# Kernel tuning notes

Measured on AMD Instinct MI355X. Metric: run time of the kernel, lower is better.

Reference implementation:

```python
import jax, jax.numpy as jnp
import numpy as np

IN_FEATURES = 2048
OUT_FEATURES = 2048
LOG_DIM = 11                      # ceil(log2(2048))
BUTTERFLY_DIM = 2 ** LOG_DIM      # 2048
MAX_BLOCKS = BUTTERFLY_DIM // 2   # 1024 (layer 0 has the most blocks)
BATCH = 16384


def setup_inputs() -> dict:
    key = jax.random.key(0)
    ks = jax.random.split(key, 5)
    x = jax.random.normal(ks[0], (BATCH, IN_FEATURES), dtype=jnp.float32)
    # Linear weights stored torch-style: [out, in]
    w_in = jax.random.normal(ks[1], (BUTTERFLY_DIM, IN_FEATURES), dtype=jnp.float32) * 0.02
    w_out = jax.random.normal(ks[2], (OUT_FEATURES, BUTTERFLY_DIM), dtype=jnp.float32) * 0.02
    b_out = jnp.zeros((OUT_FEATURES,), dtype=jnp.float32)
    # Per-stage rotation params: theta = rand*0.01, a=cos(theta), b=sin(theta).
    # Stage l uses num_blocks = BUTTERFLY_DIM // 2^(l+1) entries; pad to MAX_BLOCKS.
    theta = jax.random.uniform(ks[3], (LOG_DIM, MAX_BLOCKS), dtype=jnp.float32) * 0.01
    a_pad = jnp.cos(theta)
    b_pad = jnp.sin(theta)
    return {"x": x, "w_in": w_in, "w_out": w_out, "b_out": b_out,
            "a_pad": a_pad, "b_pad": b_pad}


def _butterfly(x, a_pad, b_pad):
    # x: [B, BUTTERFLY_DIM]
    B = x.shape[0]
    for l in range(LOG_DIM):
        block_size = 2 ** l
        num_blocks = BUTTERFLY_DIM // (2 * block_size)
        a = a_pad[l, :num_blocks][None, :, None]  # [1, nb, 1]
        b = b_pad[l, :num_blocks][None, :, None]
        xv = x.reshape(B, num_blocks, 2, block_size)
        x0 = xv[:, :, 0, :]
        x1 = xv[:, :, 1, :]
        top = a * x0 + b * x1
        bot = -b * x0 + a * x1
        x = jnp.stack([top, bot], axis=2).reshape(B, BUTTERFLY_DIM)
    return x


def reference(x, w_in, w_out, b_out, a_pad, b_pad):
    h = x @ w_in.T                      # [B, BUTTERFLY_DIM]
    h = _butterfly(h, a_pad, b_pad)
    return h @ w_out.T + b_out          # [B, OUT_FEATURES]
```

## Files before the change

kernel.cpp:

```cpp
#include <hip/hip_runtime.h>
#include <hip/hip_bf16.h>

using bf16 = __hip_bfloat16;
using bf16x8 = __attribute__((ext_vector_type(8))) __bf16;
using f32x4 = __attribute__((ext_vector_type(4))) float;

typedef const __attribute__((address_space(1))) void* gas_ptr;
typedef __attribute__((address_space(3))) void* las_ptr;
#define LOAD_LDS16(g, l) \
    __builtin_amdgcn_global_load_lds((gas_ptr)(const void*)(g), (las_ptr)(void*)(l), 16, 0, 0)

#define LOG_DIM 11
#define BDIM 2048
#define NFEAT 2048
#define BATCH 16384

__device__ __forceinline__ void cvt_chunk(const float* __restrict__ x,
                                          bf16* __restrict__ x_bf, int chunk, int tid) {
    #pragma unroll
    for (int it = 0; it < 16; ++it) {
        size_t i = ((size_t)chunk * 16 + it) * 2048 + tid * 8;
        float4 v0 = *(const float4*)(x + i);
        float4 v1 = *(const float4*)(x + i + 4);
        union { bf16 h[8]; int4 v; } u;
        u.h[0] = __float2bfloat16(v0.x); u.h[1] = __float2bfloat16(v0.y);
        u.h[2] = __float2bfloat16(v0.z); u.h[3] = __float2bfloat16(v0.w);
        u.h[4] = __float2bfloat16(v1.x); u.h[5] = __float2bfloat16(v1.y);
        u.h[6] = __float2bfloat16(v1.z); u.h[7] = __float2bfloat16(v1.w);
        *(int4*)(x_bf + i) = u.v;
    }
}

__global__ __launch_bounds__(256) void prep1(const float* __restrict__ w_out,
                                             const float* __restrict__ a_pad,
                                             const float* __restrict__ b_pad,
                                             const float* __restrict__ w_in,
                                             bf16* __restrict__ woutb,
                                             bf16* __restrict__ wint,
                                             const float* __restrict__ x,
                                             bf16* __restrict__ x_bf) {
    __shared__ float v[BDIM];
    __shared__ float tile[32][33];
    const int t = threadIdx.x;
    if (blockIdx.x < 2048) {
        const int o = blockIdx.x;
        const float* row = w_out + (size_t)o * BDIM;
        for (int i = t; i < BDIM / 4; i += 256)
            ((float4*)v)[i] = ((const float4*)row)[i];
        __syncthreads();
        for (int l = LOG_DIM - 1; l >= 0; --l) {
            #pragma unroll
            for (int pp = 0; pp < 4; ++pp) {
                int p = t + pp * 256;
                int j = p >> l;
                int s = p & ((1 << l) - 1);
                int i0 = (j << (l + 1)) | s;
                int i1 = i0 + (1 << l);
                float a = a_pad[l * (BDIM / 2) + j];
                float b = b_pad[l * (BDIM / 2) + j];
                float x0 = v[i0], x1 = v[i1];
                v[i0] = a * x0 - b * x1;
                v[i1] = b * x0 + a * x1;
            }
            __syncthreads();
        }
        union { bf16 h[8]; int4 vv; } u;
        #pragma unroll
        for (int j = 0; j < 8; ++j) u.h[j] = __float2bfloat16(v[t * 8 + j]);
        *(int4*)(woutb + (size_t)o * BDIM + t * 8) = u.vv;
    } else if (blockIdx.x < 6144) {
        const int b = blockIdx.x - 2048;
        const int bx = b & 63, by = b >> 6;
        const int tx = t & 31, ty = t >> 5;
        #pragma unroll
        for (int r = ty; r < 32; r += 8)
            tile[r][tx] = w_in[(size_t)(by * 32 + r) * NFEAT + bx * 32 + tx];
        __syncthreads();
        #pragma unroll
        for (int r = ty; r < 32; r += 8)
            wint[(size_t)(bx * 32 + r) * NFEAT + by * 32 + tx] = __float2bfloat16(tile[tx][r]);
    } else {
        cvt_chunk(x, x_bf, 768 + (blockIdx.x - 6144), t);
    }
}

__global__ __launch_bounds__(256, 2) void prep2(const bf16* __restrict__ Aw,
                                                const bf16* __restrict__ Btw,
                                                bf16* __restrict__ Cpart,
                                                const float* __restrict__ x,
                                                bf16* __restrict__ x_bf) {
    __shared__ bf16 sA[128 * 32];
    __shared__ bf16 sB[128 * 32];
    const int tid = threadIdx.x;

    if (blockIdx.x >= 1024) {
        cvt_chunk(x, x_bf, blockIdx.x - 1024, tid);
        return;
    }

    constexpr int BK = 32, LDA = 2048, KLEN = 512, NN = 2048;
    const int sk = blockIdx.x;
    const int bx = sk & 15, by = (sk >> 4) & 15, kz = sk >> 8;
    const bf16* A = Aw + kz * KLEN;
    const bf16* Bt = Btw + kz * KLEN;
    bf16* C = Cpart + (size_t)kz * NN * NN;

    const int wave = tid >> 6, lane = tid & 63;
    const int wr = wave >> 1, wc = wave & 1;
    const int mBase = by * 128, nBase = bx * 128;

    const int r0 = tid >> 2, c0 = tid & 3;
    const int r1 = (256 + tid) >> 2;

    const bf16* gA0 = A + (size_t)(mBase + r0) * LDA + c0 * 8;
    const bf16* gA1 = A + (size_t)(mBase + r1) * LDA + c0 * 8;
    const bf16* gB0 = Bt + (size_t)(nBase + r0) * LDA + c0 * 8;
    const bf16* gB1 = Bt + (size_t)(nBase + r1) * LDA + c0 * 8;

    char* lA0 = (char*)sA + (wave * 64) * 16;
    char* lA1 = (char*)sA + (256 + wave * 64) * 16;
    char* lB0 = (char*)sB + (wave * 64) * 16;
    char* lB1 = (char*)sB + (256 + wave * 64) * 16;

    f32x4 acc[4][4];
    #pragma unroll
    for (int i = 0; i < 4; ++i)
        #pragma unroll
        for (int j = 0; j < 4; ++j) acc[i][j] = (f32x4){0.f, 0.f, 0.f, 0.f};

    const int aRow = wr * 64 + (lane & 15);
    const int bRow = wc * 64 + (lane & 15);
    const int kOff = (lane >> 4) * 8;

    for (int k0 = 0; k0 < KLEN; k0 += BK) {
        LOAD_LDS16(gA0, lA0);
        LOAD_LDS16(gA1, lA1);
        LOAD_LDS16(gB0, lB0);
        LOAD_LDS16(gB1, lB1);
        gA0 += BK; gA1 += BK; gB0 += BK; gB1 += BK;
        __syncthreads();
        bf16x8 af[4], bfr[4];
        #pragma unroll
        for (int mf = 0; mf < 4; ++mf)
            af[mf] = *reinterpret_cast<const bf16x8*>(&sA[(aRow + mf * 16) * BK + kOff]);
        #pragma unroll
        for (int nf = 0; nf < 4; ++nf)
            bfr[nf] = *reinterpret_cast<const bf16x8*>(&sB[(bRow + nf * 16) * BK + kOff]);
        #pragma unroll
        for (int mf = 0; mf < 4; ++mf)
            #pragma unroll
            for (int nf = 0; nf < 4; ++nf)
                acc[mf][nf] = __builtin_amdgcn_mfma_f32_16x16x32_bf16(
                    af[mf], bfr[nf], acc[mf][nf], 0, 0, 0);
        __syncthreads();
    }

    const int cRow0 = mBase + wr * 64 + (lane >> 4) * 4;
    const int cCol0 = nBase + wc * 64 + (lane & 15);
    #pragma unroll
    for (int mf = 0; mf < 4; ++mf)
        #pragma unroll
        for (int nf = 0; nf < 4; ++nf)
            #pragma unroll
            for (int r = 0; r < 4; ++r)
                C[(size_t)(cRow0 + mf * 16 + r) * NN + cCol0 + nf * 16] =
                    __float2bfloat16(acc[mf][nf][r]);
}

__global__ __launch_bounds__(256) void addcvt4(const bf16* __restrict__ p,
                                               bf16* __restrict__ out) {
    size_t i = ((size_t)blockIdx.x * 256 + threadIdx.x) * 8;
    constexpr size_t STRIDE = (size_t)2048 * 2048;
    float s[8];
    #pragma unroll
    for (int j = 0; j < 8; ++j) s[j] = 0.f;
    #pragma unroll
    for (int z = 0; z < 4; ++z) {
        union { bf16 h[8]; int4 v; } a;
        a.v = *(const int4*)(p + z * STRIDE + i);
        #pragma unroll
        for (int j = 0; j < 8; ++j) s[j] += __bfloat162float(a.h[j]);
    }
    union { bf16 h[8]; int4 v; } o;
    #pragma unroll
    for (int j = 0; j < 8; ++j) o.h[j] = __float2bfloat16(s[j]);
    *(int4*)(out + i) = o.v;
}

#define GK 2048
#define LDS_SLOT 65536
#define LDS_BOFF 32768
#define LDS_KH 16384

__global__ __launch_bounds__(512, 2) void gemm256(const bf16* __restrict__ A,
                                                  const bf16* __restrict__ Bt,
                                                  const float* __restrict__ bias,
                                                  float* __restrict__ C) {
    __shared__ __align__(16) char lds[131072];

    const int tid = threadIdx.x;
    const int wave = tid >> 6, lane = tid & 63;
    const int l15 = lane & 15, kc = lane >> 4;
    const int wm = wave >> 2, wn = wave & 3;

    const int bid = blockIdx.x;
    const int swz = (bid & 7) * 64 + (bid >> 3);
    const int bm = swz >> 3, bn = swz & 7;
    const int mBase = bm * 256, nBase = bn * 256;

    const int c_log = tid ^ ((tid >> 3) & 3);
    const int srow = c_log >> 2, skc = c_log & 3;
    const bf16* gA = A + (size_t)(mBase + srow) * GK + skc * 8;
    const bf16* gB = Bt + (size_t)(nBase + srow) * GK + skc * 8;
    const int stgBase = wave * 1024;

    const int kcx = kc ^ ((l15 >> 1) & 3);
    const int aoff = wm * 8192 + l15 * 64 + kcx * 16;
    const int boff = LDS_BOFF + wn * 4096 + l15 * 64 + kcx * 16;

    f32x4 acc[8][4];
    #pragma unroll
    for (int i = 0; i < 8; ++i)
        #pragma unroll
        for (int j = 0; j < 4; ++j) acc[i][j] = (f32x4){0.f, 0.f, 0.f, 0.f};

    bf16x8 Af[4], Bf[4];

#define STG(GSRC, LDSC, KT, KH) do {                                        \
    const bf16* _g = (GSRC) + (KT) * 64 + (KH) * 32;                        \
    LOAD_LDS16(_g, lds + (LDSC) + stgBase);                                 \
    LOAD_LDS16(_g + (size_t)128 * GK, lds + (LDSC) + stgBase + 8192);       \
} while (0)

#define READP(SLOT, KH, MH, DOB) do {                                       \
    const int _rb = (SLOT) * LDS_SLOT + (KH) * LDS_KH;                      \
    _Pragma("unroll")                                                       \
    for (int _f = 0; _f < 4; ++_f)                                          \
        Af[_f] = *(const bf16x8*)(lds + _rb + aoff + (MH) * 4096 + _f * 1024); \
    if (DOB) {                                                              \
        _Pragma("unroll")                                                   \
        for (int _f = 0; _f < 4; ++_f)                                      \
            Bf[_f] = *(const bf16x8*)(lds + _rb + boff + _f * 1024);        \
    }                                                                       \
} while (0)

    STG(gA, 0 * LDS_SLOT + 0, 0, 0);
    STG(gB, 0 * LDS_SLOT + LDS_BOFF + 0, 0, 0);
    STG(gA, 0 * LDS_SLOT + LDS_KH, 0, 1);
    STG(gB, 0 * LDS_SLOT + LDS_BOFF + LDS_KH, 0, 1);
    STG(gA, 1 * LDS_SLOT + 0, 1, 0);
    STG(gB, 1 * LDS_SLOT + LDS_BOFF + 0, 1, 0);
    STG(gB, 1 * LDS_SLOT + LDS_BOFF + LDS_KH, 1, 1);
    asm volatile("s_waitcnt vmcnt(6)");
    __builtin_amdgcn_s_barrier();

#define PH(S, KH, MH, DOB, SGSRC, SLDS, SKT, SKH, DOVM) do {                \
    READP(S, KH, MH, DOB);                                                  \
    STG(SGSRC, SLDS, SKT, SKH);                                             \
    if (DOVM) asm volatile("s_waitcnt vmcnt(6)");                           \
    __builtin_amdgcn_sched_barrier(0);                                      \
    __builtin_amdgcn_s_barrier();                                           \
    asm volatile("s_waitcnt lgkmcnt(0)");                                   \
    __builtin_amdgcn_sched_barrier(0);                                      \
    __builtin_amdgcn_s_setprio(1);                                          \
    _Pragma("unroll")                                                       \
    for (int _mf = 0; _mf < 4; ++_mf)                                       \
        _Pragma("unroll")                                                   \
        for (int _nf = 0; _nf < 4; ++_nf)                                   \
            acc[(MH) * 4 + _mf][_nf] = __builtin_amdgcn_mfma_f32_16x16x32_bf16( \
                Af[_mf], Bf[_nf], acc[(MH) * 4 + _mf][_nf], 0, 0, 0);       \
    __builtin_amdgcn_s_setprio(0);                                          \
    __builtin_amdgcn_s_barrier();                                           \
} while (0)

    for (int it = 0; it < 16; ++it) {
        const int t0 = 2 * it;
        const int t1 = (t0 + 1) & 31, t2 = (t0 + 2) & 31, t3 = (t0 + 3) & 31;
        PH(0, 0, 0, 1, gA, 1 * LDS_SLOT + LDS_KH,            t1, 1, 0);
        PH(0, 0, 1, 0, gB, 0 * LDS_SLOT + LDS_BOFF,          t2, 0, 0);
        PH(0, 1, 0, 1, gA, 0 * LDS_SLOT + 0,                 t2, 0, 0);
        PH(0, 1, 1, 0, gB, 0 * LDS_SLOT + LDS_BOFF + LDS_KH, t2, 1, 1);
        PH(1, 0, 0, 1, gA, 0 * LDS_SLOT + LDS_KH,            t2, 1, 0);
        PH(1, 0, 1, 0, gB, 1 * LDS_SLOT + LDS_BOFF,          t3, 0, 0);
        PH(1, 1, 0, 1, gA, 1 * LDS_SLOT + 0,                 t3, 0, 0);
        PH(1, 1, 1, 0, gB, 1 * LDS_SLOT + LDS_BOFF + LDS_KH, t3, 1, 1);
    }

    const int cRow0 = mBase + wm * 128 + (lane >> 4) * 4;
    const int cCol0 = nBase + wn * 64 + l15;
    float bv[4];
    #pragma unroll
    for (int nf = 0; nf < 4; ++nf) bv[nf] = bias[cCol0 + nf * 16];
    #pragma unroll
    for (int Mf = 0; Mf < 8; ++Mf)
        #pragma unroll
        for (int nf = 0; nf < 4; ++nf)
            #pragma unroll
            for (int r = 0; r < 4; ++r)
                C[(size_t)(cRow0 + Mf * 16 + r) * GK + cCol0 + nf * 16] =
                    acc[Mf][nf][r] + bv[nf];
#undef PH
#undef READP
#undef STG
}

extern "C" void kernel_launch(void* const* d_in, const int* in_sizes, int n_in,
                              void* d_out, int out_size, void* d_ws, size_t ws_size,
                              hipStream_t stream) {
    const float* x     = (const float*)d_in[0];
    const float* w_in  = (const float*)d_in[1];
    const float* w_out = (const float*)d_in[2];
    const float* b_out = (const float*)d_in[3];
    const float* a_pad = (const float*)d_in[4];
    const float* b_pad = (const float*)d_in[5];
    float* out = (float*)d_out;

    char* ws = (char*)d_ws;
    bf16* x_bf  = (bf16*)ws;
    bf16* woutb = (bf16*)(ws + (size_t)67108864);
    bf16* wint  = (bf16*)(ws + (size_t)75497472);
    bf16* mcomb = (bf16*)(ws + (size_t)83886080);

    bf16* part = (bf16*)d_out;

    prep1<<<dim3(6400), dim3(256), 0, stream>>>(w_out, a_pad, b_pad, w_in,
                                                woutb, wint, x, x_bf);
    prep2<<<dim3(1792), dim3(256), 0, stream>>>(woutb, wint, part, x, x_bf);
    addcvt4<<<dim3(NFEAT * BDIM / (256 * 8)), dim3(256), 0, stream>>>(part, mcomb);
    gemm256<<<dim3((BATCH / 256) * (NFEAT / 256)), dim3(512), 0, stream>>>(
        x_bf, mcomb, b_out, out);
}
```

Measured before the change: 228.0 us.

## Use pipelined 256-tile split-K GEMM for weight combine, move x conversion to prep1

The weight-combination GEMM (2048x2048x2048, split-K by 4) previously ran in a simple 128-tile kernel, sharing its launch with part of the x-to-bf16 conversion. It now uses a copy of the main pipelined 256x256 MFMA kernel with a 3D grid over tiles and K-splits. All of the x conversion moves into prep1. The aim is faster MFMA throughput for the combine step, at the cost of a grid of only 256 blocks and no overlap of the conversion with that GEMM.

```diff
diff --git a/kernel.cpp b/kernel.cpp
--- a/kernel.cpp
+++ b/kernel.cpp
@@ -42,8 +42,10 @@
     __shared__ float v[BDIM];
     __shared__ float tile[32][33];
     const int t = threadIdx.x;
-    if (blockIdx.x < 2048) {
-        const int o = blockIdx.x;
+    if (blockIdx.x < 1024) {
+        cvt_chunk(x, x_bf, blockIdx.x, t);
+    } else if (blockIdx.x < 3072) {
+        const int o = blockIdx.x - 1024;
         const float* row = w_out + (size_t)o * BDIM;
         for (int i = t; i < BDIM / 4; i += 256)
             ((float4*)v)[i] = ((const float4*)row)[i];
@@ -68,8 +70,8 @@
         #pragma unroll
         for (int j = 0; j < 8; ++j) u.h[j] = __float2bfloat16(v[t * 8 + j]);
         *(int4*)(woutb + (size_t)o * BDIM + t * 8) = u.vv;
-    } else if (blockIdx.x < 6144) {
-        const int b = blockIdx.x - 2048;
+    } else {
+        const int b = blockIdx.x - 3072;
         const int bx = b & 63, by = b >> 6;
         const int tx = t & 31, ty = t >> 5;
         #pragma unroll
@@ -79,112 +81,7 @@
         #pragma unroll
         for (int r = ty; r < 32; r += 8)
             wint[(size_t)(bx * 32 + r) * NFEAT + by * 32 + tx] = __float2bfloat16(tile[tx][r]);
-    } else {
-        cvt_chunk(x, x_bf, 768 + (blockIdx.x - 6144), t);
-    }
-}
-
-__global__ __launch_bounds__(256, 2) void prep2(const bf16* __restrict__ Aw,
-                                                const bf16* __restrict__ Btw,
-                                                bf16* __restrict__ Cpart,
-                                                const float* __restrict__ x,
-                                                bf16* __restrict__ x_bf) {
-    __shared__ bf16 sA[128 * 32];
-    __shared__ bf16 sB[128 * 32];
-    const int tid = threadIdx.x;
-
-    if (blockIdx.x >= 1024) {
-        cvt_chunk(x, x_bf, blockIdx.x - 1024, tid);
-        return;
-    }
-
-    constexpr int BK = 32, LDA = 2048, KLEN = 512, NN = 2048;
-    const int sk = blockIdx.x;
-    const int bx = sk & 15, by = (sk >> 4) & 15, kz = sk >> 8;
-    const bf16* A = Aw + kz * KLEN;
-    const bf16* Bt = Btw + kz * KLEN;
-    bf16* C = Cpart + (size_t)kz * NN * NN;
-
-    const int wave = tid >> 6, lane = tid & 63;
-    const int wr = wave >> 1, wc = wave & 1;
-    const int mBase = by * 128, nBase = bx * 128;
-
-    const int r0 = tid >> 2, c0 = tid & 3;
-    const int r1 = (256 + tid) >> 2;
-
-    const bf16* gA0 = A + (size_t)(mBase + r0) * LDA + c0 * 8;
-    const bf16* gA1 = A + (size_t)(mBase + r1) * LDA + c0 * 8;
-    const bf16* gB0 = Bt + (size_t)(nBase + r0) * LDA + c0 * 8;
-    const bf16* gB1 = Bt + (size_t)(nBase + r1) * LDA + c0 * 8;
-
-    char* lA0 = (char*)sA + (wave * 64) * 16;
-    char* lA1 = (char*)sA + (256 + wave * 64) * 16;
-    char* lB0 = (char*)sB + (wave * 64) * 16;
-    char* lB1 = (char*)sB + (256 + wave * 64) * 16;
-
-    f32x4 acc[4][4];
-    #pragma unroll
-    for (int i = 0; i < 4; ++i)
-        #pragma unroll
-        for (int j = 0; j < 4; ++j) acc[i][j] = (f32x4){0.f, 0.f, 0.f, 0.f};
-
-    const int aRow = wr * 64 + (lane & 15);
-    const int bRow = wc * 64 + (lane & 15);
-    const int kOff = (lane >> 4) * 8;
-
-    for (int k0 = 0; k0 < KLEN; k0 += BK) {
-        LOAD_LDS16(gA0, lA0);
-        LOAD_LDS16(gA1, lA1);
-        LOAD_LDS16(gB0, lB0);
-        LOAD_LDS16(gB1, lB1);
-        gA0 += BK; gA1 += BK; gB0 += BK; gB1 += BK;
-        __syncthreads();
-        bf16x8 af[4], bfr[4];
-        #pragma unroll
-        for (int mf = 0; mf < 4; ++mf)
-            af[mf] = *reinterpret_cast<const bf16x8*>(&sA[(aRow + mf * 16) * BK + kOff]);
-        #pragma unroll
-        for (int nf = 0; nf < 4; ++nf)
-            bfr[nf] = *reinterpret_cast<const bf16x8*>(&sB[(bRow + nf * 16) * BK + kOff]);
-        #pragma unroll
-        for (int mf = 0; mf < 4; ++mf)
-            #pragma unroll
-            for (int nf = 0; nf < 4; ++nf)
-                acc[mf][nf] = __builtin_amdgcn_mfma_f32_16x16x32_bf16(
-                    af[mf], bfr[nf], acc[mf][nf], 0, 0, 0);
-        __syncthreads();
-    }
-
-    const int cRow0 = mBase + wr * 64 + (lane >> 4) * 4;
-    const int cCol0 = nBase + wc * 64 + (lane & 15);
-    #pragma unroll
-    for (int mf = 0; mf < 4; ++mf)
-        #pragma unroll
-        for (int nf = 0; nf < 4; ++nf)
-            #pragma unroll
-            for (int r = 0; r < 4; ++r)
-                C[(size_t)(cRow0 + mf * 16 + r) * NN + cCol0 + nf * 16] =
-                    __float2bfloat16(acc[mf][nf][r]);
-}
-
-__global__ __launch_bounds__(256) void addcvt4(const bf16* __restrict__ p,
-                                               bf16* __restrict__ out) {
-    size_t i = ((size_t)blockIdx.x * 256 + threadIdx.x) * 8;
-    constexpr size_t STRIDE = (size_t)2048 * 2048;
-    float s[8];
-    #pragma unroll
-    for (int j = 0; j < 8; ++j) s[j] = 0.f;
-    #pragma unroll
-    for (int z = 0; z < 4; ++z) {
-        union { bf16 h[8]; int4 v; } a;
-        a.v = *(const int4*)(p + z * STRIDE + i);
-        #pragma unroll
-        for (int j = 0; j < 8; ++j) s[j] += __bfloat162float(a.h[j]);
-    }
-    union { bf16 h[8]; int4 v; } o;
-    #pragma unroll
-    for (int j = 0; j < 8; ++j) o.h[j] = __float2bfloat16(s[j]);
-    *(int4*)(out + i) = o.v;
+    }
 }
 
 #define GK 2048
@@ -192,10 +89,9 @@
 #define LDS_BOFF 32768
 #define LDS_KH 16384
 
-__global__ __launch_bounds__(512, 2) void gemm256(const bf16* __restrict__ A,
-                                                  const bf16* __restrict__ Bt,
-                                                  const float* __restrict__ bias,
-                                                  float* __restrict__ C) {
+__global__ __launch_bounds__(512, 2) void gemmM_sk(const bf16* __restrict__ A,
+                                                   const bf16* __restrict__ Bt,
+                                                   bf16* __restrict__ part) {
     __shared__ __align__(16) char lds[131072];
 
     const int tid = threadIdx.x;
@@ -203,15 +99,14 @@
     const int l15 = lane & 15, kc = lane >> 4;
     const int wm = wave >> 2, wn = wave & 3;
 
-    const int bid = blockIdx.x;
-    const int swz = (bid & 7) * 64 + (bid >> 3);
-    const int bm = swz >> 3, bn = swz & 7;
-    const int mBase = bm * 256, nBase = bn * 256;
+    const int mBase = blockIdx.y * 256, nBase = blockIdx.x * 256;
+    const int kz = blockIdx.z;
+    bf16* C = part + (size_t)kz * GK * GK;
 
     const int c_log = tid ^ ((tid >> 3) & 3);
     const int srow = c_log >> 2, skc = c_log & 3;
-    const bf16* gA = A + (size_t)(mBase + srow) * GK + skc * 8;
-    const bf16* gB = Bt + (size_t)(nBase + srow) * GK + skc * 8;
+    const bf16* gA = A + (size_t)(mBase + srow) * GK + kz * 512 + skc * 8;
+    const bf16* gB = Bt + (size_t)(nBase + srow) * GK + kz * 512 + skc * 8;
     const int stgBase = wave * 1024;
 
     const int kcx = kc ^ ((l15 >> 1) & 3);
@@ -273,6 +168,135 @@
     __builtin_amdgcn_s_barrier();                                           \
 } while (0)
 
+    for (int it = 0; it < 4; ++it) {
+        const int t0 = 2 * it;
+        const int t1 = (t0 + 1) & 7, t2 = (t0 + 2) & 7, t3 = (t0 + 3) & 7;
+        PH(0, 0, 0, 1, gA, 1 * LDS_SLOT + LDS_KH,            t1, 1, 0);
+        PH(0, 0, 1, 0, gB, 0 * LDS_SLOT + LDS_BOFF,          t2, 0, 0);
+        PH(0, 1, 0, 1, gA, 0 * LDS_SLOT + 0,                 t2, 0, 0);
+        PH(0, 1, 1, 0, gB, 0 * LDS_SLOT + LDS_BOFF + LDS_KH, t2, 1, 1);
+        PH(1, 0, 0, 1, gA, 0 * LDS_SLOT + LDS_KH,            t2, 1, 0);
+        PH(1, 0, 1, 0, gB, 1 * LDS_SLOT + LDS_BOFF,          t3, 0, 0);
+        PH(1, 1, 0, 1, gA, 1 * LDS_SLOT + 0,                 t3, 0, 0);
+        PH(1, 1, 1, 0, gB, 1 * LDS_SLOT + LDS_BOFF + LDS_KH, t3, 1, 1);
+    }
+
+    const int cRow0 = mBase + wm * 128 + (lane >> 4) * 4;
+    const int cCol0 = nBase + wn * 64 + l15;
+    #pragma unroll
+    for (int Mf = 0; Mf < 8; ++Mf)
+        #pragma unroll
+        for (int nf = 0; nf < 4; ++nf)
+            #pragma unroll
+            for (int r = 0; r < 4; ++r)
+                C[(size_t)(cRow0 + Mf * 16 + r) * GK + cCol0 + nf * 16] =
+                    __float2bfloat16(acc[Mf][nf][r]);
+#undef PH
+#undef READP
+#undef STG
+}
+
+__global__ __launch_bounds__(256) void addcvt4(const bf16* __restrict__ p,
+                                               bf16* __restrict__ out) {
+    size_t i = ((size_t)blockIdx.x * 256 + threadIdx.x) * 8;
+    constexpr size_t STRIDE = (size_t)2048 * 2048;
+    float s[8];
+    #pragma unroll
+    for (int j = 0; j < 8; ++j) s[j] = 0.f;
+    #pragma unroll
+    for (int z = 0; z < 4; ++z) {
+        union { bf16 h[8]; int4 v; } a;
+        a.v = *(const int4*)(p + z * STRIDE + i);
+        #pragma unroll
+        for (int j = 0; j < 8; ++j) s[j] += __bfloat162float(a.h[j]);
+    }
+    union { bf16 h[8]; int4 v; } o;
+    #pragma unroll
+    for (int j = 0; j < 8; ++j) o.h[j] = __float2bfloat16(s[j]);
+    *(int4*)(out + i) = o.v;
+}
+
+__global__ __launch_bounds__(512, 2) void gemm256(const bf16* __restrict__ A,
+                                                  const bf16* __restrict__ Bt,
+                                                  const float* __restrict__ bias,
+                                                  float* __restrict__ C) {
+    __shared__ __align__(16) char lds[131072];
+
+    const int tid = threadIdx.x;
+    const int wave = tid >> 6, lane = tid & 63;
+    const int l15 = lane & 15, kc = lane >> 4;
+    const int wm = wave >> 2, wn = wave & 3;
+
+    const int bid = blockIdx.x;
+    const int swz = (bid & 7) * 64 + (bid >> 3);
+    const int bm = swz >> 3, bn = swz & 7;
+    const int mBase = bm * 256, nBase = bn * 256;
+
+    const int c_log = tid ^ ((tid >> 3) & 3);
+    const int srow = c_log >> 2, skc = c_log & 3;
+    const bf16* gA = A + (size_t)(mBase + srow) * GK + skc * 8;
+    const bf16* gB = Bt + (size_t)(nBase + srow) * GK + skc * 8;
+    const int stgBase = wave * 1024;
+
+    const int kcx = kc ^ ((l15 >> 1) & 3);
+    const int aoff = wm * 8192 + l15 * 64 + kcx * 16;
+    const int boff = LDS_BOFF + wn * 4096 + l15 * 64 + kcx * 16;
+
+    f32x4 acc[8][4];
+    #pragma unroll
+    for (int i = 0; i < 8; ++i)
+        #pragma unroll
+        for (int j = 0; j < 4; ++j) acc[i][j] = (f32x4){0.f, 0.f, 0.f, 0.f};
+
+    bf16x8 Af[4], Bf[4];
+
+#define STG(GSRC, LDSC, KT, KH) do {                                        \
+    const bf16* _g = (GSRC) + (KT) * 64 + (KH) * 32;                        \
+    LOAD_LDS16(_g, lds + (LDSC) + stgBase);                                 \
+    LOAD_LDS16(_g + (size_t)128 * GK, lds + (LDSC) + stgBase + 8192);       \
+} while (0)
+
+#define READP(SLOT, KH, MH, DOB) do {                                       \
+    const int _rb = (SLOT) * LDS_SLOT + (KH) * LDS_KH;                      \
+    _Pragma("unroll")                                                       \
+    for (int _f = 0; _f < 4; ++_f)                                          \
+        Af[_f] = *(const bf16x8*)(lds + _rb + aoff + (MH) * 4096 + _f * 1024); \
+    if (DOB) {                                                              \
+        _Pragma("unroll")                                                   \
+        for (int _f = 0; _f < 4; ++_f)                                      \
+            Bf[_f] = *(const bf16x8*)(lds + _rb + boff + _f * 1024);        \
+    }                                                                       \
+} while (0)
+
+    STG(gA, 0 * LDS_SLOT + 0, 0, 0);
+    STG(gB, 0 * LDS_SLOT + LDS_BOFF + 0, 0, 0);
+    STG(gA, 0 * LDS_SLOT + LDS_KH, 0, 1);
+    STG(gB, 0 * LDS_SLOT + LDS_BOFF + LDS_KH, 0, 1);
+    STG(gA, 1 * LDS_SLOT + 0, 1, 0);
+    STG(gB, 1 * LDS_SLOT + LDS_BOFF + 0, 1, 0);
+    STG(gB, 1 * LDS_SLOT + LDS_BOFF + LDS_KH, 1, 1);
+    asm volatile("s_waitcnt vmcnt(6)");
+    __builtin_amdgcn_s_barrier();
+
+#define PH(S, KH, MH, DOB, SGSRC, SLDS, SKT, SKH, DOVM) do {                \
+    READP(S, KH, MH, DOB);                                                  \
+    STG(SGSRC, SLDS, SKT, SKH);                                             \
+    if (DOVM) asm volatile("s_waitcnt vmcnt(6)");                           \
+    __builtin_amdgcn_sched_barrier(0);                                      \
+    __builtin_amdgcn_s_barrier();                                           \
+    asm volatile("s_waitcnt lgkmcnt(0)");                                   \
+    __builtin_amdgcn_sched_barrier(0);                                      \
+    __builtin_amdgcn_s_setprio(1);                                          \
+    _Pragma("unroll")                                                       \
+    for (int _mf = 0; _mf < 4; ++_mf)                                       \
+        _Pragma("unroll")                                                   \
+        for (int _nf = 0; _nf < 4; ++_nf)                                   \
+            acc[(MH) * 4 + _mf][_nf] = __builtin_amdgcn_mfma_f32_16x16x32_bf16( \
+                Af[_mf], Bf[_nf], acc[(MH) * 4 + _mf][_nf], 0, 0, 0);       \
+    __builtin_amdgcn_s_setprio(0);                                          \
+    __builtin_amdgcn_s_barrier();                                           \
+} while (0)
+
     for (int it = 0; it < 16; ++it) {
         const int t0 = 2 * it;
         const int t1 = (t0 + 1) & 31, t2 = (t0 + 2) & 31, t3 = (t0 + 3) & 31;
@@ -323,9 +347,9 @@
 
     bf16* part = (bf16*)d_out;
 
-    prep1<<<dim3(6400), dim3(256), 0, stream>>>(w_out, a_pad, b_pad, w_in,
+    prep1<<<dim3(7168), dim3(256), 0, stream>>>(w_out, a_pad, b_pad, w_in,
                                                 woutb, wint, x, x_bf);
-    prep2<<<dim3(1792), dim3(256), 0, stream>>>(woutb, wint, part, x, x_bf);
+    gemmM_sk<<<dim3(8, 8, 4), dim3(512), 0, stream>>>(woutb, wint, part);
     addcvt4<<<dim3(NFEAT * BDIM / (256 * 8)), dim3(256), 0, stream>>>(part, mcomb);
     gemm256<<<dim3((BATCH / 256) * (NFEAT / 256)), dim3(512), 0, stream>>>(
         x_bf, mcomb, b_out, out);
```

After: 226.0 us. About the same (-0.9%).
